# Optimization experiments

Measured on AMD Instinct MI355X. Metric: run time of the kernel, lower is better.

## Reference

```python
import jax, jax.numpy as jnp
import numpy as np

D_MODEL, D_STATE, BATCH, SEQ = 512, 32, 8, 4096

def _hippo(n):
    i = np.arange(n)[:, None].astype(np.float64)
    j = np.arange(n)[None, :].astype(np.float64)
    P = np.where(i > j, np.sqrt(2 * i + 1) * np.sqrt(2 * j + 1), 0.0)
    P = P + np.diag(np.arange(1, n + 1).astype(np.float64))
    return (-P).astype(np.float32)

def setup_inputs() -> dict:
    key = jax.random.key(0)
    k0, k1, k2, k3 = jax.random.split(key, 4)
    x = jax.random.normal(k0, (BATCH, SEQ, D_MODEL), dtype=jnp.float32)
    A = jnp.asarray(_hippo(D_STATE))
    B = jax.random.normal(k1, (D_STATE, D_MODEL), dtype=jnp.float32) / np.float32(np.sqrt(D_MODEL))
    C = jax.random.normal(k2, (D_MODEL, D_STATE), dtype=jnp.float32) / np.float32(np.sqrt(D_STATE))
    D = jnp.ones((D_MODEL,), dtype=jnp.float32)
    log_dt = jnp.zeros((D_MODEL,), dtype=jnp.float32)
    W_out = jax.random.normal(k3, (D_MODEL, D_MODEL), dtype=jnp.float32) / np.float32(np.sqrt(D_MODEL))
    b_out = jnp.zeros((D_MODEL,), dtype=jnp.float32)
    return {"x": x, "A": A, "B": B, "C": C, "D": D, "log_dt": log_dt, "W_out": W_out, "b_out": b_out}

def reference(x, A, B, C, D, log_dt, W_out, b_out):
    # x: (b, s, d). S4 layer with bilinear discretization and tanh recurrence.
    n = A.shape[0]
    dt = jnp.mean(jnp.clip(jnp.exp(log_dt), 1e-4, 1.0))  # scalar dt.mean()
    I = jnp.eye(n, dtype=x.dtype)
    inv_term = jnp.linalg.inv(I - 0.5 * dt * A)
    A_bar = (I + 0.5 * dt * A) @ inv_term          # (n, n)
    B_bar = dt * (inv_term @ B)                    # (n, d)
    # Precompute input projection for all timesteps (vectorized):
    uB = jnp.einsum('bsd,nd->bsn', x, B_bar)       # (b, s, n)
    s0 = jnp.zeros((x.shape[0], n), dtype=x.dtype)
    def step(state, ub_t):
        state = jnp.tanh(state @ A_bar.T + ub_t)   # (b, n)
        return state, state
    final_state, states = jax.lax.scan(step, s0, jnp.swapaxes(uB, 0, 1))
    states = jnp.swapaxes(states, 0, 1)            # (b, s, n)
    y = jnp.einsum('bsn,dn->bsd', states, C) + x * D
    y = y @ W_out.T + b_out                        # output_proj (dropout = eval identity)
    return y, final_state
```

## Files before the change

### kernel.cpp

```cpp
#include <hip/hip_runtime.h>
#include <hip/hip_bf16.h>

#define D_MODEL 512
#define D_STATE 32
#define BATCH 8
#define SEQ 4096
#define MROWS (BATCH * SEQ)
#define NBLK 1024

typedef __bf16 bf16;
typedef __bf16 bf16x4 __attribute__((ext_vector_type(4)));
typedef __bf16 bf16x8 __attribute__((ext_vector_type(8)));
typedef float f32x4 __attribute__((ext_vector_type(4)));

#define CHUNK 16
#define BURN 80
#define NCHUNK (SEQ / CHUNK)

__device__ __forceinline__ bf16x8 cvt8(const f32x4 a, const f32x4 b) {
  bf16x8 h;
  h[0] = (bf16)a[0]; h[1] = (bf16)a[1]; h[2] = (bf16)a[2]; h[3] = (bf16)a[3];
  h[4] = (bf16)b[0]; h[5] = (bf16)b[1]; h[6] = (bf16)b[2]; h[7] = (bf16)b[3];
  return h;
}

__global__ __launch_bounds__(256, 4) void k_A(
    const float* __restrict__ x, const float* __restrict__ A, const float* __restrict__ B,
    const float* __restrict__ C, const float* __restrict__ Dv, const float* __restrict__ log_dt,
    const float* __restrict__ W,
    float* __restrict__ A_bar, bf16* __restrict__ CW, bf16* __restrict__ WD,
    float* __restrict__ uB, bf16* __restrict__ xb) {
  __shared__ float Xs[32][32];
  __shared__ float srw[32 * 33];
  const int bid = blockIdx.x, t = threadIdx.x;
  const int w = t >> 6, lane = t & 63;
  const int l15 = lane & 15, kg = lane >> 4;
  float* Xf = &Xs[0][0];
  const long rowbase = (long)bid * 32;

  {
    float v0 = __expf(log_dt[t]);
    float v1 = __expf(log_dt[t + 256]);
    v0 = fminf(fmaxf(v0, 1e-4f), 1.0f);
    v1 = fminf(fmaxf(v1, 1e-4f), 1.0f);
    Xf[t] = v0 + v1;
  }
  __syncthreads();
  for (int s2 = 128; s2 > 0; s2 >>= 1) {
    if (t < s2) Xf[t] += Xf[t + s2];
    __syncthreads();
  }
  const float dtv = Xf[0] * (1.0f / 512.0f);
  __syncthreads();
  {
    const int i0 = 4 * t;
    const f32x4 av = *(const f32x4*)(A + i0);
    f32x4 mv;
#pragma unroll
    for (int q = 0; q < 4; q++) {
      const int r = (i0 + q) >> 5, c = (i0 + q) & 31;
      mv[q] = (r == c ? 1.0f : 0.0f) - 0.5f * dtv * av[q];
    }
    *(f32x4*)(Xf + i0) = mv;
  }
  __syncthreads();
  if (t < 32) {
    const int j = t;
    float xcol[32];
#pragma unroll
    for (int i = 0; i < 32; i++) {
      float s0 = 0.f, s1 = 0.f, s2 = 0.f, s3 = 0.f;
#pragma unroll
      for (int k = 0; k < 32; k += 4) {
        if (k < i)     s0 -= Xf[i * 32 + k]     * xcol[k];
        if (k + 1 < i) s1 -= Xf[i * 32 + k + 1] * xcol[k + 1];
        if (k + 2 < i) s2 -= Xf[i * 32 + k + 2] * xcol[k + 2];
        if (k + 3 < i) s3 -= Xf[i * 32 + k + 3] * xcol[k + 3];
      }
      const float num = (i == j ? 1.0f : 0.0f) + ((s0 + s1) + (s2 + s3));
      xcol[i] = (i >= j) ? num / Xf[i * 32 + i] : 0.0f;
    }
#pragma unroll
    for (int i = 0; i < 32; i++) Xs[i][j] = xcol[i];
  }

  const int m = w & 1, nf = w >> 1;
  const int arow = m * 16 + l15;
  const int brow = nf * 16 + l15;
  f32x4 acc = (f32x4)(0.0f);
  {
    const float* xp = x + (rowbase + arow) * D_MODEL + kg * 8;
    bf16* xo = xb + (rowbase + arow) * D_MODEL + kg * 8;
    const float* bp = B + brow * D_MODEL + kg * 8;
#pragma unroll
    for (int kt = 0; kt < 16; kt++) {
      const f32x4 xa = *(const f32x4*)(xp + kt * 32);
      const f32x4 xc = *(const f32x4*)(xp + kt * 32 + 4);
      const bf16x8 af = cvt8(xa, xc);
      if (nf == 0) *(bf16x8*)(xo + kt * 32) = af;
      const f32x4 b0 = *(const f32x4*)(bp + kt * 32);
      const f32x4 b1 = *(const f32x4*)(bp + kt * 32 + 4);
      const bf16x8 bh = cvt8(b0, b1);
      bf16x8 bl;
#pragma unroll
      for (int q = 0; q < 4; q++) {
        bl[q]     = (bf16)(b0[q] - (float)bh[q]);
        bl[q + 4] = (bf16)(b1[q] - (float)bh[q + 4]);
      }
      acc = __builtin_amdgcn_mfma_f32_16x16x32_bf16(af, bh, acc, 0, 0, 0);
      acc = __builtin_amdgcn_mfma_f32_16x16x32_bf16(af, bl, acc, 0, 0, 0);
    }
  }
  __syncthreads();
  if (bid == 0) {
    const int i0 = 4 * t;
    const int r = t >> 3;
    f32x4 ov;
#pragma unroll
    for (int q = 0; q < 4; q++) {
      const int c = (i0 + q) & 31;
      float s = 0.f;
#pragma unroll
      for (int k = 0; k < 32; k++) {
        const float p2 = (r == k ? 1.0f : 0.0f) + 0.5f * dtv * A[r * 32 + k];
        s = fmaf(p2, Xf[k * 32 + c], s);
      }
      ov[q] = s;
    }
    *(f32x4*)(A_bar + i0) = ov;
  }
  {
    const int col = nf * 16 + l15;
#pragma unroll
    for (int jj = 0; jj < 4; jj++)
      srw[(m * 16 + kg * 4 + jj) * 33 + col] = acc[jj];
  }
  __syncthreads();
  {
    const int n = t & 31, r0 = t >> 5;
    float u0 = 0.f, u1 = 0.f, u2 = 0.f, u3 = 0.f;
#pragma unroll
    for (int k2 = 0; k2 < 32; k2++) {
      const int k = (k2 + n) & 31;
      const float xv = Xf[n * 32 + k];
      u0 = fmaf(xv, srw[(r0)      * 33 + k], u0);
      u1 = fmaf(xv, srw[(r0 + 8)  * 33 + k], u1);
      u2 = fmaf(xv, srw[(r0 + 16) * 33 + k], u2);
      u3 = fmaf(xv, srw[(r0 + 24) * 33 + k], u3);
    }
    float* up = uB + (rowbase + r0) * D_STATE + n;
    up[0]            = dtv * u0;
    up[8 * D_STATE]  = dtv * u1;
    up[16 * D_STATE] = dtv * u2;
    up[24 * D_STATE] = dtv * u3;
  }
  if (bid >= 1 && bid <= 64) {
    const int idx = (bid - 1) * 256 + t;
    const int e = idx >> 5, n = idx & 31;
    float s = 0.f;
    for (int d = 0; d < D_MODEL; d += 4) {
      const f32x4 wv = *(const f32x4*)(W + e * D_MODEL + d);
      s = fmaf(wv[0], C[(d + 0) * D_STATE + n], s);
      s = fmaf(wv[1], C[(d + 1) * D_STATE + n], s);
      s = fmaf(wv[2], C[(d + 2) * D_STATE + n], s);
      s = fmaf(wv[3], C[(d + 3) * D_STATE + n], s);
    }
    CW[idx] = (bf16)s;
  } else if (bid >= 65 && bid <= 80) {
#pragma unroll
    for (int jj = 0; jj < 16; jj++) {
      const int i = (bid - 65) * 16384 + jj * 1024 + t * 4;
      const f32x4 wv = *(const f32x4*)(W + i);
      const f32x4 dv = *(const f32x4*)(Dv + (i & 511));
      bf16x4 h;
#pragma unroll
      for (int q = 0; q < 4; q++) h[q] = (bf16)(wv[q] * dv[q]);
      *(bf16x4*)(WD + i) = h;
    }
  }
}

__global__ void k_scan(const float* __restrict__ uB, const float* __restrict__ A_bar,
                       bf16* __restrict__ Sb, float* __restrict__ fs) {
  __shared__ float sbuf[256];
  const int t = threadIdx.x;
  const int g = t >> 5, n = t & 31;
  const int chain = blockIdx.x * 8 + g;
  const int b = chain >> 8;
  const int ch = chain & 255;
  const int cs = ch * CHUNK;
  const int t0 = cs - BURN;
  const int ce = cs + CHUNK;

  float a[32];
#pragma unroll
  for (int k = 0; k < 32; k += 4) {
    const f32x4 v = *(const f32x4*)(A_bar + n * 32 + k);
    a[k] = v[0]; a[k + 1] = v[1]; a[k + 2] = v[2]; a[k + 3] = v[3];
  }
#pragma unroll
  for (int k = 0; k < 32; k++) asm volatile("" : "+v"(a[k]));

  const float* ub = uB + (long)b * SEQ * D_STATE + n;
  bf16* sp = Sb + ((long)b * SEQ + cs) * D_STATE + n;
  float* myslot = &sbuf[g * 32];

  float s = 0.f;
  float ubuf[8], unext[8];
#pragma unroll
  for (int i = 0; i < 8; i++) {
    const int tt = t0 + i;
    ubuf[i] = (tt >= 0) ? ub[(long)tt * D_STATE] : 0.f;
  }
  for (int tg = t0; tg < ce; tg += 8) {
    const int tn = tg + 8;
#pragma unroll
    for (int i = 0; i < 8; i++) {
      const int tt = tn + i;
      unext[i] = (tt >= 0 && tt < ce) ? ub[(long)tt * D_STATE] : 0.f;
    }
#pragma unroll
    for (int i = 0; i < 8; i++) {
      const int tt = tg + i;
      myslot[n] = s;
      const f32x4 s0 = *(const f32x4*)(myslot + 0);
      const f32x4 s1 = *(const f32x4*)(myslot + 4);
      const f32x4 s2 = *(const f32x4*)(myslot + 8);
      const f32x4 s3 = *(const f32x4*)(myslot + 12);
      const f32x4 s4 = *(const f32x4*)(myslot + 16);
      const f32x4 s5 = *(const f32x4*)(myslot + 20);
      const f32x4 s6 = *(const f32x4*)(myslot + 24);
      const f32x4 s7 = *(const f32x4*)(myslot + 28);
      float acc0 = ubuf[i], acc1 = 0.f, acc2 = 0.f, acc3 = 0.f;
#pragma unroll
      for (int q = 0; q < 4; q++) {
        acc0 = fmaf(a[0 + q],  s0[q], acc0);
        acc1 = fmaf(a[4 + q],  s1[q], acc1);
        acc2 = fmaf(a[8 + q],  s2[q], acc2);
        acc3 = fmaf(a[12 + q], s3[q], acc3);
        acc0 = fmaf(a[16 + q], s4[q], acc0);
        acc1 = fmaf(a[20 + q], s5[q], acc1);
        acc2 = fmaf(a[24 + q], s6[q], acc2);
        acc3 = fmaf(a[28 + q], s7[q], acc3);
      }
      const float z = (acc0 + acc1) + (acc2 + acc3);
      const float e = __expf(2.f * z);
      const float r = __builtin_amdgcn_rcpf(e + 1.f);
      s = fmaf(-2.f, r, 1.f);
      if (tt >= cs) sp[(long)(tt - cs) * D_STATE] = (bf16)s;
    }
#pragma unroll
    for (int i = 0; i < 8; i++) ubuf[i] = unext[i];
  }
  if (ch == NCHUNK - 1) fs[b * D_STATE + n] = s;
}

__device__ __forceinline__ void stage_tile(const void* gbase, long row0, long rowStrideB,
                                           int kByte, void* lds, int w, int lane) {
#pragma unroll
  for (int j = 0; j < 2; j++) {
    const int base_off = (w << 11) + (j << 10);
    const int boff = base_off + (lane << 4);
    const int r = boff >> 6;
    const int s = (boff >> 4) & 3;
    const int cb = ((s ^ (r & 3)) << 4);
    const char* src = (const char*)gbase + (row0 + r) * rowStrideB + kByte + cb;
    __builtin_amdgcn_global_load_lds(
        (const __attribute__((address_space(1))) void*)src,
        (__attribute__((address_space(3))) void*)((char*)lds + base_off), 16, 0, 0);
  }
}

__global__ __launch_bounds__(256) void k_out(const bf16* __restrict__ xb,
                                             const bf16* __restrict__ WD,
                                             const bf16* __restrict__ Sb,
                                             const bf16* __restrict__ CW,
                                             const float* __restrict__ bias,
                                             float* __restrict__ out) {
  __shared__ bf16 As[2][128 * 32];
  __shared__ bf16 Bs[2][128 * 32];
  const int tid = threadIdx.x;
  const int w = tid >> 6, lane = tid & 63;
  const int swz = (blockIdx.x & 7) * 128 + (blockIdx.x >> 3);
  const int bm = swz >> 2, bn = swz & 3;
  const long rowbase = (long)bm * 128;
  const long colbase = (long)bn * 128;
  const int wr = w >> 1, wc = w & 1;
  const int l15 = lane & 15, kg = lane >> 4;
  const int kgs = kg ^ (l15 & 3);

  f32x4 acc[4][4];
#pragma unroll
  for (int m = 0; m < 4; m++)
#pragma unroll
    for (int n = 0; n < 4; n++) acc[m][n] = (f32x4)(0.0f);

  const int aoff = (wr * 64 + l15) * 32 + kgs * 8;
  const int boff = (wc * 64 + l15) * 32 + kgs * 8;

  auto STAGE = [&](int ti, int b) {
    if (ti < 16) {
      stage_tile(xb, rowbase, 1024, ti * 64, &As[b][0], w, lane);
      stage_tile(WD, colbase, 1024, ti * 64, &Bs[b][0], w, lane);
    } else {
      stage_tile(Sb, rowbase, 64, 0, &As[b][0], w, lane);
      stage_tile(CW, colbase, 64, 0, &Bs[b][0], w, lane);
    }
  };

  STAGE(0, 0);
  __syncthreads();
#pragma unroll 1
  for (int kt = 0; kt < 17; kt++) {
    const int cur = kt & 1;
    if (kt < 16) STAGE(kt + 1, cur ^ 1);
    bf16x8 af[4], bfr[4];
#pragma unroll
    for (int m = 0; m < 4; m++) af[m] = *(const bf16x8*)&As[cur][aoff + m * 16 * 32];
#pragma unroll
    for (int n = 0; n < 4; n++) bfr[n] = *(const bf16x8*)&Bs[cur][boff + n * 16 * 32];
#pragma unroll
    for (int m = 0; m < 4; m++)
#pragma unroll
      for (int n = 0; n < 4; n++)
        acc[m][n] = __builtin_amdgcn_mfma_f32_16x16x32_bf16(af[m], bfr[n], acc[m][n], 0, 0, 0);
    __syncthreads();
  }
#pragma unroll
  for (int n = 0; n < 4; n++) {
    const int e = (int)colbase + wc * 64 + n * 16 + l15;
    const float bv = bias[e];
#pragma unroll
    for (int m = 0; m < 4; m++) {
      const long r0 = rowbase + wr * 64 + m * 16 + kg * 4;
      const f32x4 v = acc[m][n];
#pragma unroll
      for (int jj = 0; jj < 4; jj++) out[(r0 + jj) * (long)D_MODEL + e] = v[jj] + bv;
    }
  }
}

extern "C" void kernel_launch(void* const* d_in, const int* in_sizes, int n_in,
                              void* d_out, int out_size, void* d_ws, size_t ws_size,
                              hipStream_t stream) {
  const float* x      = (const float*)d_in[0];
  const float* A      = (const float*)d_in[1];
  const float* B      = (const float*)d_in[2];
  const float* C      = (const float*)d_in[3];
  const float* Dv     = (const float*)d_in[4];
  const float* log_dt = (const float*)d_in[5];
  const float* W      = (const float*)d_in[6];
  const float* b_out  = (const float*)d_in[7];
  float* out = (float*)d_out;
  float* fs  = out + (long)MROWS * D_MODEL;

  char* ws = (char*)d_ws;
  float* A_bar = (float*)(ws + 0);
  bf16*  CW    = (bf16*)(ws + (68L << 10));
  bf16*  WD    = (bf16*)(ws + (100L << 10));
  bf16*  Sb    = (bf16*)(ws + (612L << 10));
  float* uB    = (float*)(ws + (2660L << 10));
  bf16*  xb    = (bf16*)(ws + (6756L << 10));

  k_A<<<dim3(NBLK), dim3(256), 0, stream>>>(x, A, B, C, Dv, log_dt, W,
                                            A_bar, CW, WD, uB, xb);
  k_scan<<<dim3(256), dim3(256), 0, stream>>>(uB, A_bar, Sb, fs);
  k_out<<<dim3((MROWS / 128) * (D_MODEL / 128)), dim3(256), 0, stream>>>(xb, WD, Sb, CW, b_out, out);
}
```

Before: 100.7 us.

## Split parameter precompute into tiny kernel; stop recomputing inverse in every block

The former k_A made all 1024 blocks recompute dt, the 32x32 triangular inverse and its transpose before projecting x onto B. These are now computed once by a small k_pre kernel, which also builds CW with MFMA and WD, and stores a dt-scaled inverse transpose to the workspace. A new k_uB kernel processes 64 rows per block, software-pipelines the x and B loads, and applies the stored inverse from LDS. This adds one kernel launch and a global round trip for a 4 KB matrix, in exchange for removing redundant serial work from every block.

```diff
diff --git a/kernel.cpp b/kernel.cpp
--- a/kernel.cpp
+++ b/kernel.cpp
@@ -6,7 +6,6 @@
 #define BATCH 8
 #define SEQ 4096
 #define MROWS (BATCH * SEQ)
-#define NBLK 1024
 
 typedef __bf16 bf16;
 typedef __bf16 bf16x4 __attribute__((ext_vector_type(4)));
@@ -24,152 +23,111 @@
   return h;
 }
 
-__global__ __launch_bounds__(256, 4) void k_A(
-    const float* __restrict__ x, const float* __restrict__ A, const float* __restrict__ B,
-    const float* __restrict__ C, const float* __restrict__ Dv, const float* __restrict__ log_dt,
-    const float* __restrict__ W,
-    float* __restrict__ A_bar, bf16* __restrict__ CW, bf16* __restrict__ WD,
-    float* __restrict__ uB, bf16* __restrict__ xb) {
+__global__ __launch_bounds__(256) void k_pre(
+    const float* __restrict__ A, const float* __restrict__ C, const float* __restrict__ Dv,
+    const float* __restrict__ log_dt, const float* __restrict__ W,
+    float* __restrict__ A_bar, float* __restrict__ XTs,
+    bf16* __restrict__ CW, bf16* __restrict__ WD) {
   __shared__ float Xs[32][32];
-  __shared__ float srw[32 * 33];
   const int bid = blockIdx.x, t = threadIdx.x;
-  const int w = t >> 6, lane = t & 63;
-  const int l15 = lane & 15, kg = lane >> 4;
   float* Xf = &Xs[0][0];
-  const long rowbase = (long)bid * 32;
-
-  {
-    float v0 = __expf(log_dt[t]);
-    float v1 = __expf(log_dt[t + 256]);
-    v0 = fminf(fmaxf(v0, 1e-4f), 1.0f);
-    v1 = fminf(fmaxf(v1, 1e-4f), 1.0f);
-    Xf[t] = v0 + v1;
-  }
-  __syncthreads();
-  for (int s2 = 128; s2 > 0; s2 >>= 1) {
-    if (t < s2) Xf[t] += Xf[t + s2];
+
+  if (bid == 0) {
+    {
+      float v0 = __expf(log_dt[t]);
+      float v1 = __expf(log_dt[t + 256]);
+      v0 = fminf(fmaxf(v0, 1e-4f), 1.0f);
+      v1 = fminf(fmaxf(v1, 1e-4f), 1.0f);
+      Xf[t] = v0 + v1;
+    }
     __syncthreads();
-  }
-  const float dtv = Xf[0] * (1.0f / 512.0f);
-  __syncthreads();
-  {
-    const int i0 = 4 * t;
-    const f32x4 av = *(const f32x4*)(A + i0);
-    f32x4 mv;
-#pragma unroll
-    for (int q = 0; q < 4; q++) {
-      const int r = (i0 + q) >> 5, c = (i0 + q) & 31;
-      mv[q] = (r == c ? 1.0f : 0.0f) - 0.5f * dtv * av[q];
-    }
-    *(f32x4*)(Xf + i0) = mv;
-  }
-  __syncthreads();
-  if (t < 32) {
-    const int j = t;
-    float xcol[32];
-#pragma unroll
-    for (int i = 0; i < 32; i++) {
-      float s0 = 0.f, s1 = 0.f, s2 = 0.f, s3 = 0.f;
-#pragma unroll
-      for (int k = 0; k < 32; k += 4) {
-        if (k < i)     s0 -= Xf[i * 32 + k]     * xcol[k];
-        if (k + 1 < i) s1 -= Xf[i * 32 + k + 1] * xcol[k + 1];
-        if (k + 2 < i) s2 -= Xf[i * 32 + k + 2] * xcol[k + 2];
-        if (k + 3 < i) s3 -= Xf[i * 32 + k + 3] * xcol[k + 3];
+    for (int s2 = 128; s2 > 0; s2 >>= 1) {
+      if (t < s2) Xf[t] += Xf[t + s2];
+      __syncthreads();
+    }
+    const float dtv = Xf[0] * (1.0f / 512.0f);
+    __syncthreads();
+    {
+      const int i0 = 4 * t;
+      const f32x4 av = *(const f32x4*)(A + i0);
+      f32x4 mv;
+#pragma unroll
+      for (int q = 0; q < 4; q++) {
+        const int r = (i0 + q) >> 5, c = (i0 + q) & 31;
+        mv[q] = (r == c ? 1.0f : 0.0f) - 0.5f * dtv * av[q];
       }
-      const float num = (i == j ? 1.0f : 0.0f) + ((s0 + s1) + (s2 + s3));
-      xcol[i] = (i >= j) ? num / Xf[i * 32 + i] : 0.0f;
-    }
-#pragma unroll
-    for (int i = 0; i < 32; i++) Xs[i][j] = xcol[i];
-  }
-
-  const int m = w & 1, nf = w >> 1;
-  const int arow = m * 16 + l15;
-  const int brow = nf * 16 + l15;
-  f32x4 acc = (f32x4)(0.0f);
-  {
-    const float* xp = x + (rowbase + arow) * D_MODEL + kg * 8;
-    bf16* xo = xb + (rowbase + arow) * D_MODEL + kg * 8;
-    const float* bp = B + brow * D_MODEL + kg * 8;
-#pragma unroll
+      *(f32x4*)(Xf + i0) = mv;
+    }
+    __syncthreads();
+    if (t < 32) {
+      const int j = t;
+      float xcol[32];
+#pragma unroll
+      for (int i = 0; i < 32; i++) {
+        float s0 = 0.f, s1 = 0.f, s2 = 0.f, s3 = 0.f;
+#pragma unroll
+        for (int k = 0; k < 32; k += 4) {
+          if (k < i)     s0 -= Xf[i * 32 + k]     * xcol[k];
+          if (k + 1 < i) s1 -= Xf[i * 32 + k + 1] * xcol[k + 1];
+          if (k + 2 < i) s2 -= Xf[i * 32 + k + 2] * xcol[k + 2];
+          if (k + 3 < i) s3 -= Xf[i * 32 + k + 3] * xcol[k + 3];
+        }
+        const float num = (i == j ? 1.0f : 0.0f) + ((s0 + s1) + (s2 + s3));
+        xcol[i] = (i >= j) ? num / Xf[i * 32 + i] : 0.0f;
+      }
+#pragma unroll
+      for (int i = 0; i < 32; i++) Xs[i][j] = xcol[i];
+    }
+    __syncthreads();
+    {
+      const int i0 = 4 * t;
+      const int r = t >> 3;
+      f32x4 ov;
+#pragma unroll
+      for (int q = 0; q < 4; q++) {
+        const int c = (i0 + q) & 31;
+        float s = 0.f;
+#pragma unroll
+        for (int k = 0; k < 32; k++) {
+          const float p2 = (r == k ? 1.0f : 0.0f) + 0.5f * dtv * A[r * 32 + k];
+          s = fmaf(p2, Xf[k * 32 + c], s);
+        }
+        ov[q] = s;
+      }
+      *(f32x4*)(A_bar + i0) = ov;
+    }
+#pragma unroll
+    for (int i = 0; i < 4; i++) {
+      const int idx = t + i * 256;
+      const int k = idx >> 5, n = idx & 31;
+      XTs[idx] = dtv * Xf[n * 32 + k];
+    }
+  } else if (bid <= 16) {
+    const int w = t >> 6, lane = t & 63;
+    const int l15 = lane & 15, kg = lane >> 4;
+    const int m = w & 1, nf = w >> 1;
+    const int eb = (bid - 1) * 32;
+    const float* wp = W + (long)(eb + m * 16 + l15) * D_MODEL + kg * 8;
+    const int ncol = nf * 16 + l15;
+    f32x4 acc = (f32x4)(0.0f);
+#pragma unroll 1
     for (int kt = 0; kt < 16; kt++) {
-      const f32x4 xa = *(const f32x4*)(xp + kt * 32);
-      const f32x4 xc = *(const f32x4*)(xp + kt * 32 + 4);
-      const bf16x8 af = cvt8(xa, xc);
-      if (nf == 0) *(bf16x8*)(xo + kt * 32) = af;
-      const f32x4 b0 = *(const f32x4*)(bp + kt * 32);
-      const f32x4 b1 = *(const f32x4*)(bp + kt * 32 + 4);
-      const bf16x8 bh = cvt8(b0, b1);
-      bf16x8 bl;
-#pragma unroll
-      for (int q = 0; q < 4; q++) {
-        bl[q]     = (bf16)(b0[q] - (float)bh[q]);
-        bl[q + 4] = (bf16)(b1[q] - (float)bh[q + 4]);
-      }
-      acc = __builtin_amdgcn_mfma_f32_16x16x32_bf16(af, bh, acc, 0, 0, 0);
-      acc = __builtin_amdgcn_mfma_f32_16x16x32_bf16(af, bl, acc, 0, 0, 0);
-    }
-  }
-  __syncthreads();
-  if (bid == 0) {
-    const int i0 = 4 * t;
-    const int r = t >> 3;
-    f32x4 ov;
-#pragma unroll
-    for (int q = 0; q < 4; q++) {
-      const int c = (i0 + q) & 31;
-      float s = 0.f;
-#pragma unroll
-      for (int k = 0; k < 32; k++) {
-        const float p2 = (r == k ? 1.0f : 0.0f) + 0.5f * dtv * A[r * 32 + k];
-        s = fmaf(p2, Xf[k * 32 + c], s);
-      }
-      ov[q] = s;
-    }
-    *(f32x4*)(A_bar + i0) = ov;
-  }
-  {
-    const int col = nf * 16 + l15;
+      const f32x4 w0 = *(const f32x4*)(wp + kt * 32);
+      const f32x4 w1 = *(const f32x4*)(wp + kt * 32 + 4);
+      const bf16x8 af = cvt8(w0, w1);
+      bf16x8 bf;
+#pragma unroll
+      for (int j = 0; j < 8; j++)
+        bf[j] = (bf16)C[(kt * 32 + kg * 8 + j) * D_STATE + ncol];
+      acc = __builtin_amdgcn_mfma_f32_16x16x32_bf16(af, bf, acc, 0, 0, 0);
+    }
 #pragma unroll
     for (int jj = 0; jj < 4; jj++)
-      srw[(m * 16 + kg * 4 + jj) * 33 + col] = acc[jj];
-  }
-  __syncthreads();
-  {
-    const int n = t & 31, r0 = t >> 5;
-    float u0 = 0.f, u1 = 0.f, u2 = 0.f, u3 = 0.f;
-#pragma unroll
-    for (int k2 = 0; k2 < 32; k2++) {
-      const int k = (k2 + n) & 31;
-      const float xv = Xf[n * 32 + k];
-      u0 = fmaf(xv, srw[(r0)      * 33 + k], u0);
-      u1 = fmaf(xv, srw[(r0 + 8)  * 33 + k], u1);
-      u2 = fmaf(xv, srw[(r0 + 16) * 33 + k], u2);
-      u3 = fmaf(xv, srw[(r0 + 24) * 33 + k], u3);
-    }
-    float* up = uB + (rowbase + r0) * D_STATE + n;
-    up[0]            = dtv * u0;
-    up[8 * D_STATE]  = dtv * u1;
-    up[16 * D_STATE] = dtv * u2;
-    up[24 * D_STATE] = dtv * u3;
-  }
-  if (bid >= 1 && bid <= 64) {
-    const int idx = (bid - 1) * 256 + t;
-    const int e = idx >> 5, n = idx & 31;
-    float s = 0.f;
-    for (int d = 0; d < D_MODEL; d += 4) {
-      const f32x4 wv = *(const f32x4*)(W + e * D_MODEL + d);
-      s = fmaf(wv[0], C[(d + 0) * D_STATE + n], s);
-      s = fmaf(wv[1], C[(d + 1) * D_STATE + n], s);
-      s = fmaf(wv[2], C[(d + 2) * D_STATE + n], s);
-      s = fmaf(wv[3], C[(d + 3) * D_STATE + n], s);
-    }
-    CW[idx] = (bf16)s;
-  } else if (bid >= 65 && bid <= 80) {
+      CW[(eb + m * 16 + kg * 4 + jj) * D_STATE + ncol] = (bf16)acc[jj];
+  } else {
 #pragma unroll
     for (int jj = 0; jj < 16; jj++) {
-      const int i = (bid - 65) * 16384 + jj * 1024 + t * 4;
+      const int i = (bid - 17) * 16384 + jj * 1024 + t * 4;
       const f32x4 wv = *(const f32x4*)(W + i);
       const f32x4 dv = *(const f32x4*)(Dv + (i & 511));
       bf16x4 h;
@@ -177,6 +135,85 @@
       for (int q = 0; q < 4; q++) h[q] = (bf16)(wv[q] * dv[q]);
       *(bf16x4*)(WD + i) = h;
     }
+  }
+}
+
+__global__ __launch_bounds__(256, 2) void k_uB(
+    const float* __restrict__ x, const float* __restrict__ B,
+    const float* __restrict__ XTs,
+    float* __restrict__ uB, bf16* __restrict__ xb) {
+  __shared__ float sXT[1024];
+  __shared__ float srw[64 * 33];
+  const int t = threadIdx.x, w = t >> 6, lane = t & 63;
+  const int l15 = lane & 15, kg = lane >> 4;
+  const long rowbase = (long)blockIdx.x * 64;
+
+#pragma unroll
+  for (int i = 0; i < 4; i++) sXT[t + i * 256] = XTs[t + i * 256];
+
+  const int arow = w * 16 + l15;
+  const float* xp = x + (rowbase + arow) * D_MODEL + kg * 8;
+  bf16* xo = xb + (rowbase + arow) * D_MODEL + kg * 8;
+  const float* bp0 = B + l15 * D_MODEL + kg * 8;
+  const float* bp1 = B + (16 + l15) * D_MODEL + kg * 8;
+
+  f32x4 acc0 = (f32x4)(0.0f), acc1 = (f32x4)(0.0f);
+  f32x4 cx0, cx1, cb00, cb01, cb10, cb11;
+  f32x4 nx0, nx1, nb00, nb01, nb10, nb11;
+  cx0 = *(const f32x4*)(xp);      cx1 = *(const f32x4*)(xp + 4);
+  cb00 = *(const f32x4*)(bp0);    cb01 = *(const f32x4*)(bp0 + 4);
+  cb10 = *(const f32x4*)(bp1);    cb11 = *(const f32x4*)(bp1 + 4);
+
+#pragma unroll 1
+  for (int kt = 0; kt < 16; kt++) {
+    if (kt < 15) {
+      const int o = (kt + 1) * 32;
+      nx0 = *(const f32x4*)(xp + o);    nx1 = *(const f32x4*)(xp + o + 4);
+      nb00 = *(const f32x4*)(bp0 + o);  nb01 = *(const f32x4*)(bp0 + o + 4);
+      nb10 = *(const f32x4*)(bp1 + o);  nb11 = *(const f32x4*)(bp1 + o + 4);
+    }
+    const bf16x8 af = cvt8(cx0, cx1);
+    *(bf16x8*)(xo + kt * 32) = af;
+    const bf16x8 bh0 = cvt8(cb00, cb01);
+    const bf16x8 bh1 = cvt8(cb10, cb11);
+    bf16x8 bl0, bl1;
+#pragma unroll
+    for (int q = 0; q < 4; q++) {
+      bl0[q]     = (bf16)(cb00[q] - (float)bh0[q]);
+      bl0[q + 4] = (bf16)(cb01[q] - (float)bh0[q + 4]);
+      bl1[q]     = (bf16)(cb10[q] - (float)bh1[q]);
+      bl1[q + 4] = (bf16)(cb11[q] - (float)bh1[q + 4]);
+    }
+    acc0 = __builtin_amdgcn_mfma_f32_16x16x32_bf16(af, bh0, acc0, 0, 0, 0);
+    acc0 = __builtin_amdgcn_mfma_f32_16x16x32_bf16(af, bl0, acc0, 0, 0, 0);
+    acc1 = __builtin_amdgcn_mfma_f32_16x16x32_bf16(af, bh1, acc1, 0, 0, 0);
+    acc1 = __builtin_amdgcn_mfma_f32_16x16x32_bf16(af, bl1, acc1, 0, 0, 0);
+    cx0 = nx0; cx1 = nx1;
+    cb00 = nb00; cb01 = nb01; cb10 = nb10; cb11 = nb11;
+  }
+#pragma unroll
+  for (int jj = 0; jj < 4; jj++) {
+    srw[(w * 16 + kg * 4 + jj) * 33 + l15]      = acc0[jj];
+    srw[(w * 16 + kg * 4 + jj) * 33 + 16 + l15] = acc1[jj];
+  }
+  __syncthreads();
+  {
+    const int r = t & 63, ng = t >> 6;
+    f32x4 u0 = (f32x4)(0.0f), u1 = (f32x4)(0.0f);
+#pragma unroll
+    for (int k = 0; k < 32; k++) {
+      const float sv = srw[r * 33 + k];
+      const f32x4 x0 = *(const f32x4*)&sXT[k * 32 + ng * 4];
+      const f32x4 x1 = *(const f32x4*)&sXT[k * 32 + ng * 4 + 16];
+#pragma unroll
+      for (int q = 0; q < 4; q++) {
+        u0[q] = fmaf(sv, x0[q], u0[q]);
+        u1[q] = fmaf(sv, x1[q], u1[q]);
+      }
+    }
+    float* up = uB + (rowbase + r) * D_STATE;
+    *(f32x4*)(up + ng * 4) = u0;
+    *(f32x4*)(up + ng * 4 + 16) = u1;
   }
 }
 
@@ -356,14 +393,15 @@
 
   char* ws = (char*)d_ws;
   float* A_bar = (float*)(ws + 0);
+  float* XTs   = (float*)(ws + (4L << 10));
   bf16*  CW    = (bf16*)(ws + (68L << 10));
   bf16*  WD    = (bf16*)(ws + (100L << 10));
   bf16*  Sb    = (bf16*)(ws + (612L << 10));
   float* uB    = (float*)(ws + (2660L << 10));
   bf16*  xb    = (bf16*)(ws + (6756L << 10));
 
-  k_A<<<dim3(NBLK), dim3(256), 0, stream>>>(x, A, B, C, Dv, log_dt, W,
-                                            A_bar, CW, WD, uB, xb);
+  k_pre<<<dim3(33), dim3(256), 0, stream>>>(A, C, Dv, log_dt, W, A_bar, XTs, CW, WD);
+  k_uB<<<dim3(MROWS / 64), dim3(256), 0, stream>>>(x, B, XTs, uB, xb);
   k_scan<<<dim3(256), dim3(256), 0, stream>>>(uB, A_bar, Sb, fs);
   k_out<<<dim3((MROWS / 128) * (D_MODEL / 128)), dim3(256), 0, stream>>>(xb, WD, Sb, CW, b_out, out);
 }
```

New measurement: 95.63 us. 1.05x faster.
